# Optimization experiments

Measured on AMD Instinct MI355X. Metric: run time of the kernel, lower is better.

## Reference

```python
import jax, jax.numpy as jnp
import numpy as np
from jax.scipy.linalg import solve_triangular

NUM_EMBEDDINGS = 512
EMBEDDING_DIM = 64
SPARSITY = 5
COMMITMENT_COST = 0.25


def batch_omp(data, dictionary, max_nonzero):
    """Batch OMP. data: (M, B), dictionary: (M, N). Returns coeffs (N, B)."""
    M, B = data.shape
    Dt = dictionary.T                       # (N, M)
    G = Dt @ dictionary                     # (N, N) Gram matrix
    h_bar = (Dt @ data).T                   # (B, N)
    h = h_bar
    x = jnp.zeros_like(h_bar)               # (B, N)
    L = jnp.ones((B, 1, 1), data.dtype)     # growing Cholesky factor
    mask = jnp.zeros(h_bar.shape, dtype=bool)
    I = None                                # selected atom indices (B, k)
    bidx = jnp.arange(B)
    for k in range(1, max_nonzero + 1):     # small fixed unroll (5 iters)
        index = jnp.argmax(jnp.abs(h * (~mask)), axis=1)   # (B,)
        mask = mask.at[bidx, index].set(True)
        if k > 1:
            # G[I_b, index_b] for each batch element -> (B, k-1, 1)
            G_stack = G[I, index[:, None]][..., None]
            w = solve_triangular(L, G_stack, lower=True)   # (B, k-1, 1)
            wT = jnp.swapaxes(w, 1, 2)                     # (B, 1, k-1)
            w_corner = jnp.sqrt(jnp.clip(1.0 - jnp.sum(wT ** 2, axis=2, keepdims=True), 0.0))
            top = jnp.concatenate([L, jnp.zeros((B, k - 1, 1), L.dtype)], axis=2)
            bot = jnp.concatenate([wT, w_corner], axis=2)
            L = jnp.concatenate([top, bot], axis=1)        # (B, k, k)
            I = jnp.concatenate([I, index[:, None]], axis=1)
        else:
            I = index[:, None]
        h_stack = jnp.take_along_axis(h_bar, I, axis=1)[..., None]  # (B, k, 1)
        y = solve_triangular(L, h_stack, lower=True)
        x_stack = solve_triangular(jnp.swapaxes(L, 1, 2), y, lower=False)  # (B, k, 1)
        x = x.at[bidx[:, None], I].set(x_stack[..., 0])
        beta = jnp.einsum('bk,bkn->bn', x_stack[..., 0], G[I])  # (B, N)
        h = h_bar - beta
    return x.T                              # (N, B)


def setup_inputs() -> dict:
    key = jax.random.key(0)
    k1, k2 = jax.random.split(key)
    z_e = jax.random.normal(k1, (32, EMBEDDING_DIM, 32, 32), dtype=jnp.float32)
    D = jax.random.normal(k2, (EMBEDDING_DIM, NUM_EMBEDDINGS), dtype=jnp.float32)
    D = D / jnp.linalg.norm(D, axis=0)      # column-normalized atoms (as _normalize_dictionary)
    return {"z_e": z_e, "dictionary": D}


def reference(z_e, dictionary):
    # permute BCHW -> BHWC, then flat view to (embedding_dim, -1) row-major (as torch .view)
    z_perm = jnp.transpose(z_e, (0, 2, 3, 1))          # (B, H, W, C)
    input_shape = z_perm.shape
    ze_flat = z_perm.reshape(EMBEDDING_DIM, -1)        # (M, Btokens)
    coefficients = batch_omp(ze_flat, dictionary, SPARSITY)  # (N, Btokens)
    z_dl = (dictionary @ coefficients).reshape(input_shape)
    e_latent_loss = jnp.mean((jax.lax.stop_gradient(z_dl) - z_perm) ** 2)
    dl_latent_loss = jnp.mean((z_dl - jax.lax.stop_gradient(z_perm)) ** 2)
    loss = COMMITMENT_COST * e_latent_loss + dl_latent_loss
    z_out = z_perm + jax.lax.stop_gradient(z_dl - z_perm)   # straight-through
    return (jnp.transpose(z_out, (0, 3, 1, 2)), loss, coefficients)
```

## Files before the change

### kernel.cpp

```cpp
#include <hip/hip_runtime.h>

#define B_TOTAL 32768
#define NATOM   512
#define MDIM    64
#define KS      5

__global__ void k_prep(const float* __restrict__ ze, float* __restrict__ dT,
                       const float* __restrict__ D, float* __restrict__ G,
                       float* __restrict__ acc) {
    __shared__ float lds[64][65];
    const int t = threadIdx.x;
    if (blockIdx.x < 512) {
        const int n   = blockIdx.x >> 4;
        const int hw0 = (blockIdx.x & 15) * 64;
#pragma unroll
        for (int r = 0; r < 16; ++r) {
            int id = r * 256 + t;
            int c = id >> 6, i = id & 63;
            lds[c][i] = ze[n * 65536 + c * 1024 + hw0 + i];
        }
        __syncthreads();
#pragma unroll
        for (int r = 0; r < 16; ++r) {
            int id = r * 256 + t;
            int c = id & 63, j = id >> 6;
            int hw = hw0 + j;
            int h = hw >> 5, w = hw & 31;
            int m = (n << 1) | (h >> 4);
            int b = ((h & 15) << 11) | (w << 6) | c;
            dT[m * 32768 + b] = lds[c][j];
        }
    } else {
        const int i = blockIdx.x - 512;
        float* col = &lds[0][0];
        if (t < MDIM) col[t] = D[t * NATOM + i];
        __syncthreads();
        for (int j = t; j < NATOM; j += 256) {
            float s = 0.f;
#pragma unroll
            for (int m = 0; m < MDIM; ++m) s = fmaf(col[m], D[m * NATOM + j], s);
            G[i * NATOM + j] = s;
        }
        if (i == 0 && t == 0) *acc = 0.f;
    }
}

__launch_bounds__(256, 2)
__global__ void k_omp(const float* __restrict__ data, const float* __restrict__ D,
                      const float* __restrict__ G, int* __restrict__ idx_out,
                      float* __restrict__ val_out) {
    const int t    = threadIdx.x;
    const int lane = t & 63;
    const int wv   = t >> 6;
    const int b0   = blockIdx.x * 32;

    __shared__ __align__(16) float data_s[32][68];
    __shared__ __align__(16) float stage[4][2048];

#pragma unroll
    for (int r = 0; r < 8; ++r) {
        int id = r * 256 + t;
        int m = id >> 5, bb = id & 31;
        data_s[bb][m] = data[m * B_TOTAL + b0 + bb];
    }
    __syncthreads();

    const float4* __restrict__ D4 = (const float4*)D;
    const float4* __restrict__ G4 = (const float4*)G;

    float4 acc[8][2];
#pragma unroll
    for (int bb = 0; bb < 8; ++bb) {
        acc[bb][0] = make_float4(0.f, 0.f, 0.f, 0.f);
        acc[bb][1] = make_float4(0.f, 0.f, 0.f, 0.f);
    }
    const int bwbase = wv * 8;

#pragma unroll 4
    for (int c = 0; c < 16; ++c) {
        float4 df[4][2];
#pragma unroll
        for (int mm = 0; mm < 4; ++mm) {
            df[mm][0] = D4[(c * 4 + mm) * 128 + lane];
            df[mm][1] = D4[(c * 4 + mm) * 128 + 64 + lane];
        }
#pragma unroll
        for (int bb = 0; bb < 8; ++bb) {
            const float4 dv = *(const float4*)&data_s[bwbase + bb][c * 4];
            const float dm[4] = {dv.x, dv.y, dv.z, dv.w};
#pragma unroll
            for (int mm = 0; mm < 4; ++mm) {
                acc[bb][0].x = fmaf(df[mm][0].x, dm[mm], acc[bb][0].x);
                acc[bb][0].y = fmaf(df[mm][0].y, dm[mm], acc[bb][0].y);
                acc[bb][0].z = fmaf(df[mm][0].z, dm[mm], acc[bb][0].z);
                acc[bb][0].w = fmaf(df[mm][0].w, dm[mm], acc[bb][0].w);
                acc[bb][1].x = fmaf(df[mm][1].x, dm[mm], acc[bb][1].x);
                acc[bb][1].y = fmaf(df[mm][1].y, dm[mm], acc[bb][1].y);
                acc[bb][1].z = fmaf(df[mm][1].z, dm[mm], acc[bb][1].z);
                acc[bb][1].w = fmaf(df[mm][1].w, dm[mm], acc[bb][1].w);
            }
        }
    }

    const int g = lane >> 3;
    const int p = lane & 7;
    float hb[64];
#pragma unroll
    for (int r = 0; r < 2; ++r) {
        __syncthreads();
#pragma unroll
        for (int q2 = 0; q2 < 4; ++q2) {
            int bb = r * 4 + q2;
            *(float4*)&stage[wv][q2 * 512 + 4 * lane]       = acc[bb][0];
            *(float4*)&stage[wv][q2 * 512 + 256 + 4 * lane] = acc[bb][1];
        }
        __syncthreads();
        if ((g >> 2) == r) {
#pragma unroll
            for (int q = 0; q < 16; ++q) {
                const float4 v =
                    *(const float4*)&stage[wv][(g & 3) * 512 + 32 * q + 4 * p];
                hb[4 * q + 0] = v.x;
                hb[4 * q + 1] = v.y;
                hb[4 * q + 2] = v.z;
                hb[4 * q + 3] = v.w;
            }
        }
    }

    float key[64];
#pragma unroll
    for (int e = 0; e < 64; ++e) key[e] = fabsf(hb[e]);

    unsigned msk0 = 0u, msk1 = 0u;
    int   I[KS];
    float xs[KS];
    float gsel[KS];
    float Lm[15];

#pragma unroll
    for (int k = 0; k < KS; ++k) {
        float cv[4]; int ce[4]; float ch[4];
#pragma unroll
        for (int c4 = 0; c4 < 4; ++c4) {
            cv[c4] = key[16 * c4]; ce[c4] = 16 * c4; ch[c4] = hb[16 * c4];
#pragma unroll
            for (int e = 16 * c4 + 1; e < 16 * c4 + 16; ++e) {
                bool gt = key[e] > cv[c4];
                cv[c4] = gt ? key[e] : cv[c4];
                ce[c4] = gt ? e      : ce[c4];
                ch[c4] = gt ? hb[e]  : ch[c4];
            }
        }
        float bv = cv[0]; int be = ce[0]; float bhb = ch[0];
#pragma unroll
        for (int c4 = 1; c4 < 4; ++c4) {
            bool gt = cv[c4] > bv;
            bv  = gt ? cv[c4] : bv;
            be  = gt ? ce[c4] : be;
            bhb = gt ? ch[c4] : bhb;
        }
        int bn = 32 * (be >> 2) + 4 * p + (be & 3);
#pragma unroll
        for (int off = 1; off < 8; off <<= 1) {
            float ov  = __shfl_xor(bv, off);
            int   on  = __shfl_xor(bn, off);
            float ohb = __shfl_xor(bhb, off);
            bool take = (ov > bv) || (ov == bv && on < bn);
            bv = take ? ov : bv; bn = take ? on : bn; bhb = take ? ohb : bhb;
        }
        const int nsel = bn;
        I[k]    = nsel;
        gsel[k] = bhb;

        {
            int own  = (nsel >> 2) & 7;
            int esel = ((nsel >> 5) << 2) | (nsel & 3);
            if (p == own) {
                if (esel < 32) msk0 |= 1u << esel;
                else           msk1 |= 1u << (esel - 32);
            }
        }

        if (k > 0) {
            float gk[KS - 1], w[KS - 1];
#pragma unroll
            for (int ti = 0; ti < KS - 1; ++ti)
                if (ti < k) gk[ti] = G[I[ti] * NATOM + nsel];
#pragma unroll
            for (int r = 0; r < KS - 1; ++r) {
                if (r < k) {
                    float s = gk[r];
#pragma unroll
                    for (int cc = 0; cc < KS - 1; ++cc)
                        if (cc < r) s -= Lm[r * (r + 1) / 2 + cc] * w[cc];
                    w[r] = s / Lm[r * (r + 1) / 2 + r];
                }
            }
            float s2 = 0.f;
#pragma unroll
            for (int r = 0; r < KS - 1; ++r) if (r < k) s2 += w[r] * w[r];
            float wc = sqrtf(fmaxf(0.f, 1.f - s2));
#pragma unroll
            for (int cc = 0; cc < KS - 1; ++cc)
                if (cc < k) Lm[k * (k + 1) / 2 + cc] = w[cc];
            Lm[k * (k + 1) / 2 + k] = wc;
        } else {
            Lm[0] = 1.f;
        }

        float y[KS];
#pragma unroll
        for (int r = 0; r <= k; ++r) {
            float s = gsel[r];
#pragma unroll
            for (int cc = 0; cc < r; ++cc) s -= Lm[r * (r + 1) / 2 + cc] * y[cc];
            y[r] = s / Lm[r * (r + 1) / 2 + r];
        }
#pragma unroll
        for (int r = k; r >= 0; --r) {
            float s = y[r];
#pragma unroll
            for (int cc = r + 1; cc <= k; ++cc) s -= Lm[cc * (cc + 1) / 2 + r] * xs[cc];
            xs[r] = s / Lm[r * (r + 1) / 2 + r];
        }

        if (k < KS - 1) {
#pragma unroll
            for (int q = 0; q < 16; ++q) {
                float bx = 0.f, by = 0.f, bz = 0.f, bw = 0.f;
#pragma unroll
                for (int ti = 0; ti < KS - 1; ++ti) {
                    if (ti <= k) {
                        const float4 gc = G4[I[ti] * 128 + 8 * q + p];
                        bx = fmaf(xs[ti], gc.x, bx);
                        by = fmaf(xs[ti], gc.y, by);
                        bz = fmaf(xs[ti], gc.z, bz);
                        bw = fmaf(xs[ti], gc.w, bw);
                    }
                }
                {
                    float d0 = hb[4 * q + 0] - bx;
                    float d1 = hb[4 * q + 1] - by;
                    float d2 = hb[4 * q + 2] - bz;
                    float d3 = hb[4 * q + 3] - bw;
                    const int e0 = 4 * q;
                    bool m0 = (e0 + 0 < 32) ? ((msk0 >> (e0 + 0)) & 1u) : ((msk1 >> (e0 - 32)) & 1u);
                    bool m1 = (e0 + 1 < 32) ? ((msk0 >> (e0 + 1)) & 1u) : ((msk1 >> (e0 + 1 - 32)) & 1u);
                    bool m2 = (e0 + 2 < 32) ? ((msk0 >> (e0 + 2)) & 1u) : ((msk1 >> (e0 + 2 - 32)) & 1u);
                    bool m3 = (e0 + 3 < 32) ? ((msk0 >> (e0 + 3)) & 1u) : ((msk1 >> (e0 + 3 - 32)) & 1u);
                    key[e0 + 0] = m0 ? -1.f : fabsf(d0);
                    key[e0 + 1] = m1 ? -1.f : fabsf(d1);
                    key[e0 + 2] = m2 ? -1.f : fabsf(d2);
                    key[e0 + 3] = m3 ? -1.f : fabsf(d3);
                }
            }
        }
    }

    if (p == 0) {
#pragma unroll
        for (int k = 0; k < KS; ++k) {
            idx_out[k * B_TOTAL + b0 + wv * 8 + g] = I[k];
            val_out[k * B_TOTAL + b0 + wv * 8 + g] = xs[k];
        }
    }
}

__global__ void k_post(const int* __restrict__ idx, const float* __restrict__ val,
                       float* __restrict__ coeff, const float* __restrict__ dataT,
                       const float* __restrict__ D, float* __restrict__ zout,
                       float* __restrict__ acc) {
    __shared__ float lds[64][65];
    const int t = threadIdx.x;
    if (blockIdx.x < 1024) {
        const int bblk = blockIdx.x >> 3;
        const int jc   = blockIdx.x & 7;
        const int b    = bblk * 256 + t;
        int   I[KS]; float V[KS];
#pragma unroll
        for (int k = 0; k < KS; ++k) {
            I[k] = idx[k * B_TOTAL + b];
            V[k] = val[k * B_TOTAL + b];
        }
        const int j0 = jc * 64;
#pragma unroll 4
        for (int j = j0; j < j0 + 64; ++j) {
            float w = 0.f;
#pragma unroll
            for (int k = 0; k < KS; ++k) w = (I[k] == j) ? V[k] : w;
            coeff[j * B_TOTAL + b] = w;
        }
    } else {
        const int blk = blockIdx.x - 1024;
        const int n   = blk >> 4;
        const int hw0 = (blk & 15) * 64;
        float sq = 0.f;
#pragma unroll
        for (int r = 0; r < 16; ++r) {
            int id = r * 256 + t;
            int c = id & 63, j = id >> 6;
            int f = n * 65536 + (hw0 + j) * 64 + c;
            int b = f & 32767;
            int m = f >> 15;
            float zdl = 0.f;
#pragma unroll
            for (int k = 0; k < KS; ++k) {
                int   a = idx[k * B_TOTAL + b];
                float v = val[k * B_TOTAL + b];
                zdl = fmaf(v, D[m * NATOM + a], zdl);
            }
            float zp   = dataT[f];
            float diff = zdl - zp;
            lds[c][j] = zp + diff;
            sq = fmaf(diff, diff, sq);
        }
        __syncthreads();
#pragma unroll
        for (int r = 0; r < 16; ++r) {
            int id = r * 256 + t;
            int cc = id >> 6, i = id & 63;
            zout[n * 65536 + cc * 1024 + hw0 + i] = lds[cc][i];
        }
#pragma unroll
        for (int off = 32; off > 0; off >>= 1) sq += __shfl_xor(sq, off);
        __shared__ float red[4];
        if ((t & 63) == 0) red[t >> 6] = sq;
        __syncthreads();
        if (t == 0) atomicAdd(acc, red[0] + red[1] + red[2] + red[3]);
    }
}

__global__ void k_loss(const float* __restrict__ acc, float* __restrict__ out_loss) {
    if (threadIdx.x == 0 && blockIdx.x == 0)
        *out_loss = 1.25f * (*acc / 2097152.f);
}

extern "C" void kernel_launch(void* const* d_in, const int* in_sizes, int n_in,
                              void* d_out, int out_size, void* d_ws, size_t ws_size,
                              hipStream_t stream) {
    const float* ze = (const float*)d_in[0];
    const float* D  = (const float*)d_in[1];

    float* G     = (float*)d_ws;
    int*   idxp  = (int*)  ((char*)d_ws + (size_t)262144 * 4);
    float* valp  = (float*)((char*)d_ws + (size_t)(262144 + 163840) * 4);
    float* accp  = (float*)((char*)d_ws + (size_t)(262144 + 2 * 163840) * 4);
    float* dataT = (float*)((char*)d_ws + (size_t)(262144 + 2 * 163840 + 64) * 4);

    float* zout  = (float*)d_out;
    float* lossp = zout + 2097152;
    float* coeff = zout + 2097153;

    k_prep<<<1024, 256, 0, stream>>>(ze, dataT, D, G, accp);
    k_omp <<<1024, 256, 0, stream>>>(dataT, D, G, idxp, valp);
    k_post<<<1536, 256, 0, stream>>>(idxp, valp, coeff, dataT, D, zout, accp);
    k_loss<<<1, 64, 0, stream>>>(accp, lossp);
}
```

Before: 180.6 us.

## Drop transposed data buffer and fold loss finalize into post kernel

New measurement: 198.9 us. 10.1% more time.

```diff
diff --git a/kernel.cpp b/kernel.cpp
--- a/kernel.cpp
+++ b/kernel.cpp
@@ -5,48 +5,24 @@
 #define MDIM    64
 #define KS      5
 
-__global__ void k_prep(const float* __restrict__ ze, float* __restrict__ dT,
-                       const float* __restrict__ D, float* __restrict__ G,
+__global__ void k_gram(const float* __restrict__ D, float* __restrict__ G,
                        float* __restrict__ acc) {
-    __shared__ float lds[64][65];
+    const int i = blockIdx.x;
     const int t = threadIdx.x;
-    if (blockIdx.x < 512) {
-        const int n   = blockIdx.x >> 4;
-        const int hw0 = (blockIdx.x & 15) * 64;
-#pragma unroll
-        for (int r = 0; r < 16; ++r) {
-            int id = r * 256 + t;
-            int c = id >> 6, i = id & 63;
-            lds[c][i] = ze[n * 65536 + c * 1024 + hw0 + i];
-        }
-        __syncthreads();
-#pragma unroll
-        for (int r = 0; r < 16; ++r) {
-            int id = r * 256 + t;
-            int c = id & 63, j = id >> 6;
-            int hw = hw0 + j;
-            int h = hw >> 5, w = hw & 31;
-            int m = (n << 1) | (h >> 4);
-            int b = ((h & 15) << 11) | (w << 6) | c;
-            dT[m * 32768 + b] = lds[c][j];
-        }
-    } else {
-        const int i = blockIdx.x - 512;
-        float* col = &lds[0][0];
-        if (t < MDIM) col[t] = D[t * NATOM + i];
-        __syncthreads();
-        for (int j = t; j < NATOM; j += 256) {
-            float s = 0.f;
-#pragma unroll
-            for (int m = 0; m < MDIM; ++m) s = fmaf(col[m], D[m * NATOM + j], s);
-            G[i * NATOM + j] = s;
-        }
-        if (i == 0 && t == 0) *acc = 0.f;
-    }
+    __shared__ float col[MDIM];
+    if (t < MDIM) col[t] = D[t * NATOM + i];
+    __syncthreads();
+    for (int j = t; j < NATOM; j += 256) {
+        float s = 0.f;
+#pragma unroll
+        for (int m = 0; m < MDIM; ++m) s = fmaf(col[m], D[m * NATOM + j], s);
+        G[i * NATOM + j] = s;
+    }
+    if (i == 0 && t == 0) { acc[0] = 0.f; ((unsigned*)acc)[1] = 0u; }
 }
 
 __launch_bounds__(256, 2)
-__global__ void k_omp(const float* __restrict__ data, const float* __restrict__ D,
+__global__ void k_omp(const float* __restrict__ ze, const float* __restrict__ D,
                       const float* __restrict__ G, int* __restrict__ idx_out,
                       float* __restrict__ val_out) {
     const int t    = threadIdx.x;
@@ -57,11 +33,18 @@
     __shared__ __align__(16) float data_s[32][68];
     __shared__ __align__(16) float stage[4][2048];
 
-#pragma unroll
-    for (int r = 0; r < 8; ++r) {
-        int id = r * 256 + t;
-        int m = id >> 5, bb = id & 31;
-        data_s[bb][m] = data[m * B_TOTAL + b0 + bb];
+    {
+        const int cbase = b0 & 32;
+        const int w_f   = (b0 >> 6) & 31;
+        const int h_lo  = (b0 >> 11) << 5;
+#pragma unroll
+        for (int r = 0; r < 8; ++r) {
+            int id = r * 256 + t;
+            int m = id >> 5, bb = id & 31;
+            int addr = (m >> 1) * 65536 + (cbase + bb) * 1024
+                     + ((m & 1) << 9) + h_lo + w_f;
+            data_s[bb][m] = ze[addr];
+        }
     }
     __syncthreads();
 
@@ -268,9 +251,9 @@
 }
 
 __global__ void k_post(const int* __restrict__ idx, const float* __restrict__ val,
-                       float* __restrict__ coeff, const float* __restrict__ dataT,
+                       float* __restrict__ coeff, const float* __restrict__ ze,
                        const float* __restrict__ D, float* __restrict__ zout,
-                       float* __restrict__ acc) {
+                       float* __restrict__ acc, float* __restrict__ out_loss) {
     __shared__ float lds[64][65];
     const int t = threadIdx.x;
     if (blockIdx.x < 1024) {
@@ -310,7 +293,7 @@
                 float v = val[k * B_TOTAL + b];
                 zdl = fmaf(v, D[m * NATOM + a], zdl);
             }
-            float zp   = dataT[f];
+            float zp   = ze[n * 65536 + c * 1024 + hw0 + j];
             float diff = zdl - zp;
             lds[c][j] = zp + diff;
             sq = fmaf(diff, diff, sq);
@@ -327,13 +310,16 @@
         __shared__ float red[4];
         if ((t & 63) == 0) red[t >> 6] = sq;
         __syncthreads();
-        if (t == 0) atomicAdd(acc, red[0] + red[1] + red[2] + red[3]);
-    }
-}
-
-__global__ void k_loss(const float* __restrict__ acc, float* __restrict__ out_loss) {
-    if (threadIdx.x == 0 && blockIdx.x == 0)
-        *out_loss = 1.25f * (*acc / 2097152.f);
+        if (t == 0) {
+            atomicAdd(acc, red[0] + red[1] + red[2] + red[3]);
+            __threadfence();
+            unsigned prev = atomicAdd(((unsigned*)acc) + 1, 1u);
+            if (prev == 511u) {
+                float a = atomicAdd(acc, 0.f);
+                out_loss[0] = 1.25f * (a / 2097152.f);
+            }
+        }
+    }
 }
 
 extern "C" void kernel_launch(void* const* d_in, const int* in_sizes, int n_in,
@@ -346,14 +332,12 @@
     int*   idxp  = (int*)  ((char*)d_ws + (size_t)262144 * 4);
     float* valp  = (float*)((char*)d_ws + (size_t)(262144 + 163840) * 4);
     float* accp  = (float*)((char*)d_ws + (size_t)(262144 + 2 * 163840) * 4);
-    float* dataT = (float*)((char*)d_ws + (size_t)(262144 + 2 * 163840 + 64) * 4);
 
     float* zout  = (float*)d_out;
     float* lossp = zout + 2097152;
     float* coeff = zout + 2097153;
 
-    k_prep<<<1024, 256, 0, stream>>>(ze, dataT, D, G, accp);
-    k_omp <<<1024, 256, 0, stream>>>(dataT, D, G, idxp, valp);
-    k_post<<<1536, 256, 0, stream>>>(idxp, valp, coeff, dataT, D, zout, accp);
-    k_loss<<<1, 64, 0, stream>>>(accp, lossp);
+    k_gram<<< 512, 256, 0, stream>>>(D, G, accp);
+    k_omp <<<1024, 256, 0, stream>>>(ze, D, G, idxp, valp);
+    k_post<<<1536, 256, 0, stream>>>(idxp, valp, coeff, ze, D, zout, accp, lossp);
 }
```
